# Performance work log

Measured on AMD Instinct MI355X. Metric: run time of the kernel, lower is better.

The kernel has to match this reference:

```python
import jax, jax.numpy as jnp
import numpy as np

H, D, EPS = 4, 16, 1e-5
N_NODES, N_EDGES, F_IN, HID, N_GRAPHS, N_CLASSES = 100000, 1600000, 128, 64, 512, 10


def _bn(x, g, b, m, v):
    # BatchNorm1d in eval mode: running stats
    return (x - m) * jax.lax.rsqrt(v + EPS) * g + b


def _tconv(x, src, dst, wq, bq, wk, bk, wv, bv, ws, bs):
    # PyG TransformerConv: q from dst node, k/v from src node, scatter-softmax over dst,
    # scatter-add aggregation, concat heads, plus root (skip) linear. Dropout=eval (identity).
    N = x.shape[0]
    q = (x @ wq + bq).reshape(N, H, D)
    k = (x @ wk + bk).reshape(N, H, D)
    v = (x @ wv + bv).reshape(N, H, D)
    alpha = (q[dst] * k[src]).sum(-1) * np.float32(1.0 / np.sqrt(D))  # [E, H]
    amax = jax.ops.segment_max(alpha, dst, num_segments=N)            # [N, H]
    amax = jnp.where(jnp.isfinite(amax), amax, 0.0)
    ex = jnp.exp(alpha - amax[dst])
    denom = jax.ops.segment_sum(ex, dst, num_segments=N)
    attn = ex / (denom[dst] + 1e-16)                                  # [E, H]
    agg = jax.ops.segment_sum(attn[:, :, None] * v[src], dst, num_segments=N)  # [N, H, D]
    return agg.reshape(N, H * D) + x @ ws + bs


def setup_inputs() -> dict:
    key = jax.random.key(0)
    ks = list(jax.random.split(key, 40))
    def w(i, shape):
        return jax.random.normal(ks[i], shape, jnp.float32) * 0.05
    inp = {}
    inp['x'] = jax.random.normal(ks[0], (N_NODES, F_IN), jnp.float32)
    inp['edge_index'] = jax.random.randint(ks[1], (2, N_EDGES), 0, N_NODES, dtype=jnp.int32)
    inp['batch'] = jnp.sort(jax.random.randint(ks[2], (N_NODES,), 0, N_GRAPHS, dtype=jnp.int32))
    i = 3
    for p, fin in (('c1', F_IN), ('c2', HID)):
        for nm in ('wq', 'wk', 'wv', 'ws'):
            inp[p + '_' + nm] = w(i, (fin, HID)); i += 1
            inp[p + '_b' + nm[1]] = w(i, (HID,)); i += 1
    for p in ('bn1', 'bn2', 'clbn'):
        inp[p + '_g'] = jnp.ones((HID,), jnp.float32)
        inp[p + '_b'] = jnp.zeros((HID,), jnp.float32)
        inp[p + '_m'] = jnp.zeros((HID,), jnp.float32)
        inp[p + '_v'] = jnp.ones((HID,), jnp.float32)
    for nm, shp in (('p1_w', (HID, HID)), ('p2_w', (HID, HID)), ('cl1_w', (HID, HID)), ('cl2_w', (HID, N_CLASSES))):
        inp[nm] = w(i, shp); i += 1
    inp['p1_b'] = jnp.zeros((HID,), jnp.float32)
    inp['p2_b'] = jnp.zeros((HID,), jnp.float32)
    inp['cl1_b'] = jnp.zeros((HID,), jnp.float32)
    inp['cl2_b'] = jnp.zeros((N_CLASSES,), jnp.float32)
    return inp


def reference(x, edge_index, batch,
              c1_wq, c1_bq, c1_wk, c1_bk, c1_wv, c1_bv, c1_ws, c1_bs,
              bn1_g, bn1_b, bn1_m, bn1_v,
              c2_wq, c2_bq, c2_wk, c2_bk, c2_wv, c2_bv, c2_ws, c2_bs,
              bn2_g, bn2_b, bn2_m, bn2_v,
              p1_w, p1_b, p2_w, p2_b,
              cl1_w, cl1_b, clbn_g, clbn_b, clbn_m, clbn_v, cl2_w, cl2_b):
    src, dst = edge_index[0], edge_index[1]
    h = _tconv(x, src, dst, c1_wq, c1_bq, c1_wk, c1_bk, c1_wv, c1_bv, c1_ws, c1_bs)
    h = jax.nn.relu(_bn(h, bn1_g, bn1_b, bn1_m, bn1_v))
    h = _tconv(h, src, dst, c2_wq, c2_bq, c2_wk, c2_bk, c2_wv, c2_bv, c2_ws, c2_bs)
    h = jax.nn.relu(_bn(h, bn2_g, bn2_b, bn2_m, bn2_v))
    g = jax.ops.segment_max(h, batch, num_segments=N_GRAPHS)  # global_max_pool [G, HID]
    g = jnp.where(jnp.isfinite(g), g, 0.0)
    g = jax.nn.relu(g @ p1_w + p1_b) @ p2_w + p2_b
    g = jax.nn.relu(_bn(g @ cl1_w + cl1_b, clbn_g, clbn_b, clbn_m, clbn_v))
    logits = g @ cl2_w + cl2_b
    return jax.nn.log_softmax(logits, axis=1)
```

## Files before the change

kernel.cpp:

```cpp
#include <hip/hip_runtime.h>
#include <hip/hip_bf16.h>
#include <math.h>

constexpr int NN = 100000;
constexpr int EE = 1600000;
constexpr int GG = 512;
constexpr int MPAD = 100096;
constexpr int NBUCK = 782;
constexpr int EPB = 8192;
constexpr int CAP = 4096;

typedef __attribute__((ext_vector_type(8))) short short8;
typedef __attribute__((ext_vector_type(4))) float floatx4;

__device__ __forceinline__ unsigned short f2bf_rne(float f) {
    unsigned int u = __float_as_uint(f);
    u += 0x7fff + ((u >> 16) & 1);
    return (unsigned short)(u >> 16);
}
__device__ __forceinline__ float bf_lo(unsigned int u) { return __uint_as_float(u << 16); }
__device__ __forceinline__ float bf_hi(unsigned int u) { return __uint_as_float(u & 0xffff0000u); }

template<int C>
__device__ __forceinline__ float dppadd(float x) {
    int t = __builtin_amdgcn_update_dpp(0, __float_as_int(x), C, 0xf, 0xf, true);
    return x + __int_as_float(t);
}
__device__ __forceinline__ float qred4(float p) {
    p = dppadd<0xB1>(p);
    p = dppadd<0x4E>(p);
    return p;
}

__device__ __forceinline__ float dot4(uint2 kd, float q0, float q1, float q2, float q3) {
    return fmaf(bf_lo(kd.x), q0, fmaf(bf_hi(kd.x), q1,
           fmaf(bf_lo(kd.y), q2, bf_hi(kd.y) * q3)));
}

__global__ __launch_bounds__(512) void k_part(const int* __restrict__ src,
                                              const int* __restrict__ dst,
                                              int* __restrict__ bcur,
                                              unsigned int* __restrict__ ppair) {
    __shared__ int cnt[NBUCK];
    __shared__ int base[NBUCK];
    int tid = threadIdx.x;
    int e0 = blockIdx.x * EPB;
    for (int j = tid; j < NBUCK; j += 512) cnt[j] = 0;
    __syncthreads();
    int myd[16], myr[16];
    #pragma unroll
    for (int t = 0; t < 16; t++) {
        int i = e0 + t * 512 + tid;
        if (i < EE) {
            int d = dst[i];
            myd[t] = d;
            myr[t] = atomicAdd(&cnt[d >> 7], 1);
        } else myd[t] = -1;
    }
    __syncthreads();
    for (int j = tid; j < NBUCK; j += 512) base[j] = atomicAdd(&bcur[j], cnt[j]);
    __syncthreads();
    #pragma unroll
    for (int t = 0; t < 16; t++) {
        int i = e0 + t * 512 + tid;
        if (myd[t] >= 0) {
            int b = myd[t] >> 7;
            int pos = base[b] + myr[t];
            if (pos < CAP)
                ppair[(size_t)b * CAP + pos] =
                    ((unsigned int)src[i] << 7) | (unsigned int)(myd[t] & 127);
        }
    }
}

__global__ __launch_bounds__(256) void k_bucket(const unsigned int* __restrict__ ppair,
                                                const int* __restrict__ bcur,
                                                int* __restrict__ rowbeg,
                                                int* __restrict__ rowend,
                                                int* __restrict__ csr) {
    __shared__ int cnt[128];
    __shared__ int sa[128], sb[128];
    __shared__ int cur[128];
    int t = threadIdx.x;
    int b = blockIdx.x;
    int n = bcur[b]; if (n > CAP) n = CAP;
    int start = b * CAP;
    if (t < 128) cnt[t] = 0;
    __syncthreads();
    for (int i = t; i < n; i += 256)
        atomicAdd(&cnt[ppair[start + i] & 127], 1);
    __syncthreads();
    if (t < 128) sa[t] = cnt[t];
    __syncthreads();
    int* p = sa; int* q = sb;
    for (int off = 1; off < 128; off <<= 1) {
        if (t < 128) q[t] = (t >= off) ? (p[t] + p[t - off]) : p[t];
        __syncthreads();
        int* tmp = p; p = q; q = tmp;
    }
    if (t < 128) {
        int excl = (t == 0) ? 0 : p[t - 1];
        rowbeg[b * 128 + t] = start + excl;
        rowend[b * 128 + t] = start + p[t];
        cur[t] = start + excl;
    }
    __syncthreads();
    for (int i = t; i < n; i += 256) {
        unsigned int e = ppair[start + i];
        int pos = atomicAdd(&cur[e & 127], 1);
        csr[pos] = (int)(e >> 7);
    }
}

__global__ __launch_bounds__(256) void k_cvt_all(
    const float* __restrict__ w1q, const float* __restrict__ b1q,
    const float* __restrict__ w1k, const float* __restrict__ b1k,
    const float* __restrict__ w1v, const float* __restrict__ b1v,
    const float* __restrict__ w1s, const float* __restrict__ b1s,
    const float* __restrict__ w2q, const float* __restrict__ b2q,
    const float* __restrict__ w2k, const float* __restrict__ b2k,
    const float* __restrict__ w2v, const float* __restrict__ b2v,
    const float* __restrict__ w2s, const float* __restrict__ b2s,
    unsigned short* __restrict__ Bt1, float* __restrict__ bias1,
    unsigned short* __restrict__ Bt2, float* __restrict__ bias2,
    float* __restrict__ g0) {
    int b = blockIdx.x, tid = threadIdx.x;
    if (b < 128) {
        g0[b * 256 + tid] = 0.f;
        int idx = b * 256 + tid;
        int col = idx >> 7, k = idx & 127;
        float val;
        if (col < 64)        val = w1k[k * 64 + col];
        else if (col < 128)  val = w1v[k * 64 + (col - 64)];
        else if (col < 192)  val = w1q[k * 64 + (col - 128)];
        else                 val = w1s[k * 64 + (col - 192)];
        Bt1[col * 128 + k] = f2bf_rne(val);
        if (k == 0) {
            float bv;
            if (col < 64)        bv = b1k[col];
            else if (col < 128)  bv = b1v[col - 64];
            else if (col < 192)  bv = b1q[col - 128];
            else                 bv = b1s[col - 192];
            bias1[col] = bv;
        }
    } else {
        int idx = (b - 128) * 256 + tid;
        int col = idx >> 6, k = idx & 63;
        float val;
        if (col < 64)        val = w2k[k * 64 + col];
        else if (col < 128)  val = w2v[k * 64 + (col - 64)];
        else if (col < 192)  val = w2q[k * 64 + (col - 128)];
        else                 val = w2s[k * 64 + (col - 192)];
        Bt2[col * 64 + k] = f2bf_rne(val);
        if (k == 0) {
            float bv;
            if (col < 64)        bv = b2k[col];
            else if (col < 128)  bv = b2v[col - 64];
            else if (col < 192)  bv = b2q[col - 128];
            else                 bv = b2s[col - 192];
            bias2[col] = bv;
        }
    }
}

template<int K, bool AF32>
__global__ __launch_bounds__(256) void gemm_mfma(
    const void* __restrict__ Araw,
    const unsigned short* __restrict__ Bt,
    const float* __restrict__ bias,
    unsigned short* __restrict__ out0,
    unsigned short* __restrict__ out1) {
    constexpr int SP = 72;
    __shared__ short As[128 * SP];
    int tid = threadIdx.x;
    int wave = tid >> 6, lane = tid & 63;
    int wm = wave >> 1, wn = wave & 1;
    int quad = lane >> 4, l16 = lane & 15;
    int rowBase = blockIdx.x * 128;
    int ct = blockIdx.y;

    const unsigned short* bRow[4];
    #pragma unroll
    for (int j = 0; j < 4; j++)
        bRow[j] = Bt + (size_t)(ct * 128 + wn * 64 + j * 16 + l16) * K + quad * 8;

    floatx4 acc[4][4];
    #pragma unroll
    for (int i = 0; i < 4; i++)
        #pragma unroll
        for (int j = 0; j < 4; j++) acc[i][j] = (floatx4)0.f;

    for (int kc = 0; kc < K; kc += 64) {
        #pragma unroll
        for (int it = 0; it < 4; it++) {
            int flat = it * 256 + tid;
            int r = flat >> 3, c8 = (flat & 7) * 8;
            int ar = rowBase + r; if (ar >= NN) ar = NN - 1;
            short8 va;
            if constexpr (AF32) {
                const float* ap = (const float*)Araw + (size_t)ar * K + kc + c8;
                float4 u0 = *reinterpret_cast<const float4*>(ap);
                float4 u1 = *reinterpret_cast<const float4*>(ap + 4);
                va[0] = (short)f2bf_rne(u0.x); va[1] = (short)f2bf_rne(u0.y);
                va[2] = (short)f2bf_rne(u0.z); va[3] = (short)f2bf_rne(u0.w);
                va[4] = (short)f2bf_rne(u1.x); va[5] = (short)f2bf_rne(u1.y);
                va[6] = (short)f2bf_rne(u1.z); va[7] = (short)f2bf_rne(u1.w);
            } else {
                va = *reinterpret_cast<const short8*>(
                        (const unsigned short*)Araw + (size_t)ar * K + kc + c8);
            }
            *reinterpret_cast<short8*>(&As[r * SP + c8]) = va;
        }
        __syncthreads();
        #pragma unroll
        for (int ks = 0; ks < 2; ks++) {
            short8 af[4], bf[4];
            #pragma unroll
            for (int i = 0; i < 4; i++)
                af[i] = *reinterpret_cast<const short8*>(&As[(wm * 64 + i * 16 + l16) * SP + ks * 32 + quad * 8]);
            #pragma unroll
            for (int j = 0; j < 4; j++)
                bf[j] = *reinterpret_cast<const short8*>(bRow[j] + kc + ks * 32);
            #pragma unroll
            for (int i = 0; i < 4; i++)
                #pragma unroll
                for (int j = 0; j < 4; j++)
                    acc[i][j] = __builtin_amdgcn_mfma_f32_16x16x32_bf16(af[i], bf[j], acc[i][j], 0, 0, 0);
        }
        __syncthreads();
    }

    unsigned short* outp = ct ? out1 : out0;
    float bj[4];
    #pragma unroll
    for (int j = 0; j < 4; j++) bj[j] = bias[ct * 128 + wn * 64 + j * 16 + l16];
    #pragma unroll
    for (int i = 0; i < 4; i++) {
        #pragma unroll
        for (int j = 0; j < 4; j++) {
            int col = wn * 64 + j * 16 + l16;
            #pragma unroll
            for (int r = 0; r < 4; r++) {
                int row = rowBase + wm * 64 + i * 16 + quad * 4 + r;
                if (row < NN)
                    outp[(size_t)row * 128 + col] = f2bf_rne(acc[i][j][r] + bj[j]);
            }
        }
    }
}

__global__ __launch_bounds__(256) void attn_fused(
    const unsigned short* __restrict__ qsb,
    const uint2* __restrict__ kvp,
    const int* __restrict__ rowbeg,
    const int* __restrict__ rowend,
    const int* __restrict__ csr,
    const float* __restrict__ bng, const float* __restrict__ bnb,
    const float* __restrict__ bnm, const float* __restrict__ bnv,
    uint2* __restrict__ h_out) {
    int wid = (blockIdx.x * 256 + threadIdx.x) >> 6;
    int lane = threadIdx.x & 63;
    if (wid >= NN) return;
    int g = lane >> 4, ql = lane & 15;
    const uint2* qrow = reinterpret_cast<const uint2*>(qsb + (size_t)wid * 128);
    const float SC = 0.3606737602222409f;
    uint2 qd = qrow[ql];
    float q0 = bf_lo(qd.x) * SC, q1 = bf_hi(qd.x) * SC;
    float q2 = bf_lo(qd.y) * SC, q3 = bf_hi(qd.y) * SC;
    int jb = rowbeg[wid], je = rowend[wid];
    float a0 = 0.f, a1 = 0.f, a2 = 0.f, a3 = 0.f, denom = 0.f;
    int j = jb;
    for (; j + 7 < je; j += 8) {
        int sA = csr[j + g];
        int sB = csr[j + 4 + g];
        const uint2* rA = kvp + (size_t)sA * 32;
        const uint2* rB = kvp + (size_t)sB * 32;
        uint2 kA = rA[ql], vA = rA[16 + ql];
        uint2 kB = rB[ql], vB = rB[16 + ql];
        float pA = qred4(dot4(kA, q0, q1, q2, q3));
        float pB = qred4(dot4(kB, q0, q1, q2, q3));
        float eA = exp2f(pA), eB = exp2f(pB);
        denom += eA + eB;
        a0 = fmaf(eA, bf_lo(vA.x), a0);
        a1 = fmaf(eA, bf_hi(vA.x), a1);
        a2 = fmaf(eA, bf_lo(vA.y), a2);
        a3 = fmaf(eA, bf_hi(vA.y), a3);
        a0 = fmaf(eB, bf_lo(vB.x), a0);
        a1 = fmaf(eB, bf_hi(vB.x), a1);
        a2 = fmaf(eB, bf_lo(vB.y), a2);
        a3 = fmaf(eB, bf_hi(vB.y), a3);
    }
    for (; j < je; j += 4) {
        int jj = j + g;
        bool valid = jj < je;
        int s = csr[valid ? jj : je - 1];
        const uint2* r = kvp + (size_t)s * 32;
        uint2 kd = r[ql], vd = r[16 + ql];
        float p = qred4(dot4(kd, q0, q1, q2, q3));
        float e = valid ? exp2f(p) : 0.f;
        denom += e;
        a0 = fmaf(e, bf_lo(vd.x), a0);
        a1 = fmaf(e, bf_hi(vd.x), a1);
        a2 = fmaf(e, bf_lo(vd.y), a2);
        a3 = fmaf(e, bf_hi(vd.y), a3);
    }
    a0 += __shfl_xor(a0, 16);  a0 += __shfl_xor(a0, 32);
    a1 += __shfl_xor(a1, 16);  a1 += __shfl_xor(a1, 32);
    a2 += __shfl_xor(a2, 16);  a2 += __shfl_xor(a2, 32);
    a3 += __shfl_xor(a3, 16);  a3 += __shfl_xor(a3, 32);
    denom += __shfl_xor(denom, 16);  denom += __shfl_xor(denom, 32);
    float inv = 1.f / (denom + 1e-16f);
    uint2 sd = qrow[16 + ql];
    float4 m4 = reinterpret_cast<const float4*>(bnm)[ql];
    float4 v4 = reinterpret_cast<const float4*>(bnv)[ql];
    float4 g4 = reinterpret_cast<const float4*>(bng)[ql];
    float4 b4 = reinterpret_cast<const float4*>(bnb)[ql];
    float o0 = a0 * inv + bf_lo(sd.x), o1 = a1 * inv + bf_hi(sd.x);
    float o2 = a2 * inv + bf_lo(sd.y), o3 = a3 * inv + bf_hi(sd.y);
    o0 = fmaxf((o0 - m4.x) * rsqrtf(v4.x + 1e-5f) * g4.x + b4.x, 0.f);
    o1 = fmaxf((o1 - m4.y) * rsqrtf(v4.y + 1e-5f) * g4.y + b4.y, 0.f);
    o2 = fmaxf((o2 - m4.z) * rsqrtf(v4.z + 1e-5f) * g4.z + b4.z, 0.f);
    o3 = fmaxf((o3 - m4.w) * rsqrtf(v4.w + 1e-5f) * g4.w + b4.w, 0.f);
    if (g == 0) {
        uint2 hw;
        hw.x = (unsigned int)f2bf_rne(o0) | ((unsigned int)f2bf_rne(o1) << 16);
        hw.y = (unsigned int)f2bf_rne(o2) | ((unsigned int)f2bf_rne(o3) << 16);
        h_out[(size_t)wid * 16 + ql] = hw;
    }
}

__global__ __launch_bounds__(256) void k_pool(const unsigned short* __restrict__ h,
                                              const int* __restrict__ batch,
                                              float* __restrict__ g0) {
    int f = threadIdx.x & 63;
    int sub = threadIdx.x >> 6;
    int n0 = blockIdx.x * 128;
    int nEnd = n0 + 128; if (nEnd > NN) nEnd = NN;
    int cur_g = -1; float cur_m = 0.f;
    for (int n = n0 + sub; n < nEnd; n += 4) {
        int bg = batch[n];
        float val = __uint_as_float((unsigned int)h[(size_t)n * 64 + f] << 16);
        if (bg != cur_g) {
            if (cur_g >= 0) atomicMax((int*)&g0[cur_g * 64 + f], __float_as_int(cur_m));
            cur_g = bg; cur_m = val;
        } else {
            cur_m = fmaxf(cur_m, val);
        }
    }
    if (cur_g >= 0) atomicMax((int*)&g0[cur_g * 64 + f], __float_as_int(cur_m));
}

__global__ __launch_bounds__(256) void k_mlp(
    const float* __restrict__ g0,
    const float* __restrict__ p1w, const float* __restrict__ p1b,
    const float* __restrict__ p2w, const float* __restrict__ p2b,
    const float* __restrict__ cl1w, const float* __restrict__ cl1b,
    const float* __restrict__ bg, const float* __restrict__ bb,
    const float* __restrict__ bm, const float* __restrict__ bv,
    const float* __restrict__ cl2w, const float* __restrict__ cl2b,
    float* __restrict__ outp) {
    __shared__ float w1[64 * 64], w2[64 * 64], w3[64 * 64], w4[64 * 10];
    __shared__ float sb1[64], sb2[64], sb3[64], sbn[4 * 64], sb4[10];
    int tid = threadIdx.x;
    for (int i = tid; i < 64 * 64; i += 256) { w1[i] = p1w[i]; w2[i] = p2w[i]; w3[i] = cl1w[i]; }
    for (int i = tid; i < 64 * 10; i += 256) w4[i] = cl2w[i];
    if (tid < 64) {
        sb1[tid] = p1b[tid]; sb2[tid] = p2b[tid]; sb3[tid] = cl1b[tid];
        sbn[tid] = bg[tid]; sbn[64 + tid] = bb[tid];
        sbn[128 + tid] = bm[tid]; sbn[192 + tid] = bv[tid];
    }
    if (tid < 10) sb4[tid] = cl2b[tid];
    __syncthreads();
    int lane = tid & 63, w = tid >> 6;
    int row = blockIdx.x * 4 + w;
    float x = g0[row * 64 + lane];
    if (!isfinite(x)) x = 0.f;
    float a = sb1[lane];
    for (int k = 0; k < 64; k++) a += __shfl(x, k) * w1[k * 64 + lane];
    x = fmaxf(a, 0.f);
    a = sb2[lane];
    for (int k = 0; k < 64; k++) a += __shfl(x, k) * w2[k * 64 + lane];
    x = a;
    a = sb3[lane];
    for (int k = 0; k < 64; k++) a += __shfl(x, k) * w3[k * 64 + lane];
    a = (a - sbn[128 + lane]) * rsqrtf(sbn[192 + lane] + 1e-5f) * sbn[lane] + sbn[64 + lane];
    x = fmaxf(a, 0.f);
    float lg[10];
    #pragma unroll
    for (int c = 0; c < 10; c++) {
        float p = x * w4[lane * 10 + c];
        p += __shfl_xor(p, 1);  p += __shfl_xor(p, 2);  p += __shfl_xor(p, 4);
        p += __shfl_xor(p, 8);  p += __shfl_xor(p, 16); p += __shfl_xor(p, 32);
        lg[c] = p + sb4[c];
    }
    float mx = lg[0];
    #pragma unroll
    for (int c = 1; c < 10; c++) mx = fmaxf(mx, lg[c]);
    float s = 0.f;
    #pragma unroll
    for (int c = 0; c < 10; c++) s += __expf(lg[c] - mx);
    float lse = mx + logf(s);
    float o = 0.f;
    #pragma unroll
    for (int c = 0; c < 10; c++) if (lane == c) o = lg[c];
    if (lane < 10) outp[row * 10 + lane] = o - lse;
}

extern "C" void kernel_launch(void* const* d_in, const int* in_sizes, int n_in,
                              void* d_out, int out_size, void* d_ws, size_t ws_size,
                              hipStream_t stream) {
    const float* x     = (const float*)d_in[0];
    const int*   ei    = (const int*)d_in[1];
    const int*   batch = (const int*)d_in[2];
    const float *c1_wq = (const float*)d_in[3],  *c1_bq = (const float*)d_in[4];
    const float *c1_wk = (const float*)d_in[5],  *c1_bk = (const float*)d_in[6];
    const float *c1_wv = (const float*)d_in[7],  *c1_bv = (const float*)d_in[8];
    const float *c1_ws = (const float*)d_in[9],  *c1_bs = (const float*)d_in[10];
    const float *c2_wq = (const float*)d_in[11], *c2_bq = (const float*)d_in[12];
    const float *c2_wk = (const float*)d_in[13], *c2_bk = (const float*)d_in[14];
    const float *c2_wv = (const float*)d_in[15], *c2_bv = (const float*)d_in[16];
    const float *c2_ws = (const float*)d_in[17], *c2_bs = (const float*)d_in[18];
    const float *bn1_g = (const float*)d_in[19], *bn1_b = (const float*)d_in[20];
    const float *bn1_m = (const float*)d_in[21], *bn1_v = (const float*)d_in[22];
    const float *bn2_g = (const float*)d_in[23], *bn2_b = (const float*)d_in[24];
    const float *bn2_m = (const float*)d_in[25], *bn2_v = (const float*)d_in[26];
    const float *clbn_g = (const float*)d_in[27], *clbn_b = (const float*)d_in[28];
    const float *clbn_m = (const float*)d_in[29], *clbn_v = (const float*)d_in[30];
    const float *p1_w = (const float*)d_in[31], *p2_w = (const float*)d_in[32];
    const float *cl1_w = (const float*)d_in[33], *cl2_w = (const float*)d_in[34];
    const float *p1_b = (const float*)d_in[35], *p2_b = (const float*)d_in[36];
    const float *cl1_b = (const float*)d_in[37], *cl2_b = (const float*)d_in[38];

    char* ws = (char*)d_ws;
    unsigned short* kv     = (unsigned short*)(ws);
    unsigned short* qsb    = (unsigned short*)(ws + 25600000);
    unsigned short* hbuf   = (unsigned short*)(ws + 51200000);
    unsigned int*   ppair  = (unsigned int*)(ws + 64012288);
    int*            csr    = (int*)(ws + 76824576);
    int*            rowbeg = (int*)(ws + 89636864);
    int*            rowend = (int*)(ws + 90037248);
    int*            bcur   = (int*)(ws + 90437632);
    float*          g0     = (float*)(ws + 90440768);
    unsigned short* Bt1    = (unsigned short*)(ws + 90571840);
    float*          b1     = (float*)(ws + 90637376);
    unsigned short* Bt2    = (unsigned short*)(ws + 90638400);
    float*          b2     = (float*)(ws + 90671168);

    const int* srcIdx = ei;
    const int* dstIdx = ei + EE;

    hipMemsetAsync(bcur, 0, NBUCK * sizeof(int), stream);

    k_cvt_all<<<192, 256, 0, stream>>>(c1_wq, c1_bq, c1_wk, c1_bk, c1_wv, c1_bv,
                                       c1_ws, c1_bs,
                                       c2_wq, c2_bq, c2_wk, c2_bk, c2_wv, c2_bv,
                                       c2_ws, c2_bs, Bt1, b1, Bt2, b2, g0);

    constexpr int PBLK = (EE + EPB - 1) / EPB;
    k_part<<<PBLK, 512, 0, stream>>>(srcIdx, dstIdx, bcur, ppair);
    k_bucket<<<NBUCK, 256, 0, stream>>>(ppair, bcur, rowbeg, rowend, csr);

    {
        dim3 grid(MPAD / 128, 2);
        gemm_mfma<128, true><<<grid, 256, 0, stream>>>(x, Bt1, b1, kv, qsb);
    }
    attn_fused<<<NN / 4, 256, 0, stream>>>(qsb, (const uint2*)kv, rowbeg, rowend, csr,
                                           bn1_g, bn1_b, bn1_m, bn1_v, (uint2*)hbuf);

    {
        dim3 grid(MPAD / 128, 2);
        gemm_mfma<64, false><<<grid, 256, 0, stream>>>(hbuf, Bt2, b2, kv, qsb);
    }
    attn_fused<<<NN / 4, 256, 0, stream>>>(qsb, (const uint2*)kv, rowbeg, rowend, csr,
                                           bn2_g, bn2_b, bn2_m, bn2_v, (uint2*)hbuf);

    k_pool<<<(NN + 127) / 128, 256, 0, stream>>>(hbuf, batch, g0);
    k_mlp<<<GG / 4, 256, 0, stream>>>(g0, p1_w, p1_b, p2_w, p2_b, cl1_w, cl1_b,
                                      clbn_g, clbn_b, clbn_m, clbn_v, cl2_w, cl2_b,
                                      (float*)d_out);
}
```

Baseline: 411.3 us.

## Widen GEMM to full 256-column tile with LDS-staged B and 32-bit gather offsets

The GEMM now computes all 256 output columns per block with 512 threads (8 waves). The weight matrix B is staged through shared memory instead of being read directly from global memory by each wave, and the A tile is loaded once rather than twice across a two-column-tile grid. This cuts redundant A reads and fp32-to-bf16 conversions, at the cost of more LDS per block and a larger block, which can lower occupancy. Separately, the attention gather computes byte offsets as 32-bit unsigned values rather than 64-bit pointer arithmetic, which trims address computation.

New measurement: 402.4 us. -2.2%, faster.

```diff
diff --git a/kernel.cpp b/kernel.cpp
--- a/kernel.cpp
+++ b/kernel.cpp
@@ -164,7 +164,7 @@
 }
 
 template<int K, bool AF32>
-__global__ __launch_bounds__(256) void gemm_mfma(
+__global__ __launch_bounds__(512) void gemm_mfma(
     const void* __restrict__ Araw,
     const unsigned short* __restrict__ Bt,
     const float* __restrict__ bias,
@@ -172,17 +172,12 @@
     unsigned short* __restrict__ out1) {
     constexpr int SP = 72;
     __shared__ short As[128 * SP];
+    __shared__ short Bs[256 * SP];
     int tid = threadIdx.x;
     int wave = tid >> 6, lane = tid & 63;
-    int wm = wave >> 1, wn = wave & 1;
+    int wm = wave >> 2, wn = wave & 3;
     int quad = lane >> 4, l16 = lane & 15;
     int rowBase = blockIdx.x * 128;
-    int ct = blockIdx.y;
-
-    const unsigned short* bRow[4];
-    #pragma unroll
-    for (int j = 0; j < 4; j++)
-        bRow[j] = Bt + (size_t)(ct * 128 + wn * 64 + j * 16 + l16) * K + quad * 8;
 
     floatx4 acc[4][4];
     #pragma unroll
@@ -192,8 +187,8 @@
 
     for (int kc = 0; kc < K; kc += 64) {
         #pragma unroll
-        for (int it = 0; it < 4; it++) {
-            int flat = it * 256 + tid;
+        for (int it = 0; it < 2; it++) {
+            int flat = it * 512 + tid;
             int r = flat >> 3, c8 = (flat & 7) * 8;
             int ar = rowBase + r; if (ar >= NN) ar = NN - 1;
             short8 va;
@@ -211,6 +206,13 @@
             }
             *reinterpret_cast<short8*>(&As[r * SP + c8]) = va;
         }
+        #pragma unroll
+        for (int it = 0; it < 4; it++) {
+            int flat = it * 512 + tid;
+            int r = flat >> 3, c8 = (flat & 7) * 8;
+            short8 vb = *reinterpret_cast<const short8*>(Bt + (size_t)r * K + kc + c8);
+            *reinterpret_cast<short8*>(&Bs[r * SP + c8]) = vb;
+        }
         __syncthreads();
         #pragma unroll
         for (int ks = 0; ks < 2; ks++) {
@@ -220,7 +222,7 @@
                 af[i] = *reinterpret_cast<const short8*>(&As[(wm * 64 + i * 16 + l16) * SP + ks * 32 + quad * 8]);
             #pragma unroll
             for (int j = 0; j < 4; j++)
-                bf[j] = *reinterpret_cast<const short8*>(bRow[j] + kc + ks * 32);
+                bf[j] = *reinterpret_cast<const short8*>(&Bs[(wn * 64 + j * 16 + l16) * SP + ks * 32 + quad * 8]);
             #pragma unroll
             for (int i = 0; i < 4; i++)
                 #pragma unroll
@@ -230,15 +232,16 @@
         __syncthreads();
     }
 
-    unsigned short* outp = ct ? out1 : out0;
+    unsigned short* outp = (wn < 2) ? out0 : out1;
+    int colBase = (wn & 1) * 64;
     float bj[4];
     #pragma unroll
-    for (int j = 0; j < 4; j++) bj[j] = bias[ct * 128 + wn * 64 + j * 16 + l16];
+    for (int j = 0; j < 4; j++) bj[j] = bias[wn * 64 + j * 16 + l16];
     #pragma unroll
     for (int i = 0; i < 4; i++) {
         #pragma unroll
         for (int j = 0; j < 4; j++) {
-            int col = wn * 64 + j * 16 + l16;
+            int col = colBase + j * 16 + l16;
             #pragma unroll
             for (int r = 0; r < 4; r++) {
                 int row = rowBase + wm * 64 + i * 16 + quad * 4 + r;
@@ -251,7 +254,7 @@
 
 __global__ __launch_bounds__(256) void attn_fused(
     const unsigned short* __restrict__ qsb,
-    const uint2* __restrict__ kvp,
+    const unsigned char* __restrict__ kvb,
     const int* __restrict__ rowbeg,
     const int* __restrict__ rowend,
     const int* __restrict__ csr,
@@ -262,6 +265,7 @@
     int lane = threadIdx.x & 63;
     if (wid >= NN) return;
     int g = lane >> 4, ql = lane & 15;
+    unsigned int qb8 = (unsigned int)(ql << 3);
     const uint2* qrow = reinterpret_cast<const uint2*>(qsb + (size_t)wid * 128);
     const float SC = 0.3606737602222409f;
     uint2 qd = qrow[ql];
@@ -271,12 +275,12 @@
     float a0 = 0.f, a1 = 0.f, a2 = 0.f, a3 = 0.f, denom = 0.f;
     int j = jb;
     for (; j + 7 < je; j += 8) {
-        int sA = csr[j + g];
-        int sB = csr[j + 4 + g];
-        const uint2* rA = kvp + (size_t)sA * 32;
-        const uint2* rB = kvp + (size_t)sB * 32;
-        uint2 kA = rA[ql], vA = rA[16 + ql];
-        uint2 kB = rB[ql], vB = rB[16 + ql];
+        unsigned int oA = ((unsigned int)csr[j + g] << 8) + qb8;
+        unsigned int oB = ((unsigned int)csr[j + 4 + g] << 8) + qb8;
+        uint2 kA = *reinterpret_cast<const uint2*>(kvb + oA);
+        uint2 vA = *reinterpret_cast<const uint2*>(kvb + oA + 128);
+        uint2 kB = *reinterpret_cast<const uint2*>(kvb + oB);
+        uint2 vB = *reinterpret_cast<const uint2*>(kvb + oB + 128);
         float pA = qred4(dot4(kA, q0, q1, q2, q3));
         float pB = qred4(dot4(kB, q0, q1, q2, q3));
         float eA = exp2f(pA), eB = exp2f(pB);
@@ -293,9 +297,9 @@
     for (; j < je; j += 4) {
         int jj = j + g;
         bool valid = jj < je;
-        int s = csr[valid ? jj : je - 1];
-        const uint2* r = kvp + (size_t)s * 32;
-        uint2 kd = r[ql], vd = r[16 + ql];
+        unsigned int o = ((unsigned int)csr[valid ? jj : je - 1] << 8) + qb8;
+        uint2 kd = *reinterpret_cast<const uint2*>(kvb + o);
+        uint2 vd = *reinterpret_cast<const uint2*>(kvb + o + 128);
         float p = qred4(dot4(kd, q0, q1, q2, q3));
         float e = valid ? exp2f(p) : 0.f;
         denom += e;
@@ -460,18 +464,14 @@
     k_part<<<PBLK, 512, 0, stream>>>(srcIdx, dstIdx, bcur, ppair);
     k_bucket<<<NBUCK, 256, 0, stream>>>(ppair, bcur, rowbeg, rowend, csr);
 
-    {
-        dim3 grid(MPAD / 128, 2);
-        gemm_mfma<128, true><<<grid, 256, 0, stream>>>(x, Bt1, b1, kv, qsb);
-    }
-    attn_fused<<<NN / 4, 256, 0, stream>>>(qsb, (const uint2*)kv, rowbeg, rowend, csr,
+    gemm_mfma<128, true><<<MPAD / 128, 512, 0, stream>>>(x, Bt1, b1, kv, qsb);
+    attn_fused<<<NN / 4, 256, 0, stream>>>(qsb, (const unsigned char*)kv,
+                                           rowbeg, rowend, csr,
                                            bn1_g, bn1_b, bn1_m, bn1_v, (uint2*)hbuf);
 
-    {
-        dim3 grid(MPAD / 128, 2);
-        gemm_mfma<64, false><<<grid, 256, 0, stream>>>(hbuf, Bt2, b2, kv, qsb);
-    }
-    attn_fused<<<NN / 4, 256, 0, stream>>>(qsb, (const uint2*)kv, rowbeg, rowend, csr,
+    gemm_mfma<64, false><<<MPAD / 128, 512, 0, stream>>>(hbuf, Bt2, b2, kv, qsb);
+    attn_fused<<<NN / 4, 256, 0, stream>>>(qsb, (const unsigned char*)kv,
+                                           rowbeg, rowend, csr,
                                            bn2_g, bn2_b, bn2_m, bn2_v, (uint2*)hbuf);
 
     k_pool<<<(NN + 127) / 128, 256, 0, stream>>>(hbuf, batch, g0);
```
